# Optimization experiments

Hardware: AMD Instinct MI355X
Metric: run time of the kernel (lower is better)

## Reference

```python
import jax, jax.numpy as jnp
import numpy as np

RES = 64

TRI_TABLE = jnp.array([
    [-1,-1,-1,-1,-1,-1],[1,0,2,-1,-1,-1],[4,0,3,-1,-1,-1],[1,4,2,1,3,4],
    [3,1,5,-1,-1,-1],[2,3,0,2,5,3],[1,4,0,1,5,4],[4,2,5,-1,-1,-1],
    [4,5,2,-1,-1,-1],[4,1,0,4,5,1],[3,2,0,3,5,2],[1,3,5,-1,-1,-1],
    [4,1,2,4,3,1],[3,0,4,-1,-1,-1],[2,0,1,-1,-1,-1],[-1,-1,-1,-1,-1,-1]], dtype=jnp.int32)
NUM_TRI = jnp.array([0,1,1,2,1,2,2,1,1,2,2,1,2,1,1,0], dtype=jnp.int32)
BASE_EDGES = jnp.array([0,1,0,2,0,3,1,2,1,3,2,3], dtype=jnp.int32)


def _make_tet_grid(res):
    # Kuhn 6-tet decomposition of each cube of a (res+1)^3 grid.
    n = res + 1
    ii, jj, kk = np.meshgrid(np.arange(n), np.arange(n), np.arange(n), indexing='ij')
    verts = (np.stack([ii, jj, kk], -1).reshape(-1, 3).astype(np.float32)) / res
    def vid(i, j, k):
        return (i * n + j) * n + k
    i, j, k = np.meshgrid(np.arange(res), np.arange(res), np.arange(res), indexing='ij')
    i, j, k = i.ravel(), j.ravel(), k.ravel()
    c = [vid(i + (b & 1), j + ((b >> 1) & 1), k + ((b >> 2) & 1)) for b in range(8)]
    kuhn = [(0,1,3,7),(0,3,2,7),(0,2,6,7),(0,6,4,7),(0,4,5,7),(0,5,1,7)]
    tets = np.stack([np.stack([c[a], c[b], c[d], c[e]], -1) for (a, b, d, e) in kuhn], 1)
    return verts, tets.reshape(-1, 4).astype(np.int64)


def setup_inputs() -> dict:
    key = jax.random.key(0)
    verts, tets = _make_tet_grid(RES)
    level = jax.random.normal(key, (verts.shape[0], 1), dtype=jnp.float32)
    return {"level": level, "pos": jnp.asarray(verts), "tet": jnp.asarray(tets), "threshold": 0}


def reference(level, pos, tet, threshold):
    sdf = level - threshold                    # [N,1]
    occ = sdf[:, 0] > 0                        # [N]
    occ_fx4 = occ[tet]                         # [F,4]
    occ_sum = occ_fx4.sum(-1)
    valid = (occ_sum > 0) & (occ_sum < 4)
    vt = tet[valid]                            # [Fv,4]
    occ_valid = occ_fx4[valid]                 # [Fv,4]

    edges = jnp.sort(vt[:, BASE_EDGES].reshape(-1, 2), axis=1)   # [Fv*6,2]
    unique_edges, idx_map = jnp.unique(edges, axis=0, return_inverse=True)
    idx_map = idx_map.reshape(-1)
    mask_edges = occ[unique_edges].sum(-1) == 1                  # crossing edges
    mapping = jnp.where(mask_edges, jnp.cumsum(mask_edges) - 1, -1)
    idx_map = mapping[idx_map].reshape(-1, 6)                    # [Fv,6]
    interp_v = unique_edges[mask_edges]                          # [M,2]

    p = pos[interp_v]                                            # [M,2,3]
    s = sdf[interp_v][..., 0] * jnp.array([1.0, -1.0], dtype=sdf.dtype)  # [M,2]
    w = s[:, ::-1] / s.sum(1, keepdims=True)                     # flip / denom
    verts_out = (p * w[..., None]).sum(1)                        # [M,3]

    v_id = 2 ** jnp.arange(4, dtype=jnp.int32)
    tetindex = (occ_valid.astype(jnp.int32) * v_id).sum(-1)      # [Fv]
    num_tri = NUM_TRI[tetindex]
    m1, m2 = num_tri == 1, num_tri == 2
    f1 = jnp.take_along_axis(idx_map[m1], TRI_TABLE[tetindex[m1]][:, :3], axis=1).reshape(-1, 3)
    f2 = jnp.take_along_axis(idx_map[m2], TRI_TABLE[tetindex[m2]][:, :6], axis=1).reshape(-1, 3)
    faces = jnp.concatenate([f1, f2], axis=0)
    return verts_out, faces
```

## Files before the change

kernel.cpp:

```cpp
#include <hip/hip_runtime.h>


#define RESX 64
#define NV   65
#define NV2  4225
#define NVERT 274625
#define BLOCK 256
#define NGE 4225
#define NGC 4096
#define NB1I 1024
#define NBND 129
#define NBLK1 1057
#define CBLK 1024
#define NFB 33
#define STAGE 9216
#define M21 0x1fffffu
#define NTRI_PACK 0x16696994u

__constant__ int c_tri[16][6] = {
    {-1,-1,-1,-1,-1,-1},{1,0,2,-1,-1,-1},{4,0,3,-1,-1,-1},{1,4,2,1,3,4},
    {3,1,5,-1,-1,-1},{2,3,0,2,5,3},{1,4,0,1,5,4},{4,2,5,-1,-1,-1},
    {4,5,2,-1,-1,-1},{4,1,0,4,5,1},{3,2,0,3,5,2},{1,3,5,-1,-1,-1},
    {4,1,2,4,3,1},{3,0,4,-1,-1,-1},{2,0,1,-1,-1,-1},{-1,-1,-1,-1,-1,-1}};
__constant__ int c_kuhn[6][4] = {{0,1,3,7},{0,3,2,7},{0,2,6,7},{0,6,4,7},{0,4,5,7},{0,5,1,7}};
__constant__ int c_off8[8] = {0,4225,65,4290,1,4226,66,4291};
__constant__ int c_loc[6][6] = {
    {0,0,0,1,1,3},{0,0,0,2,3,2},{0,0,0,2,2,6},
    {0,0,0,4,6,4},{0,0,0,4,4,5},{0,0,0,1,5,1}};
__constant__ int c_dir[6][6] = {
    {3,5,6,1,2,0},{5,1,6,3,0,4},{1,2,6,0,4,3},
    {2,0,6,1,3,5},{0,4,6,3,5,1},{4,3,6,0,1,2}};

typedef unsigned long long u64;

__device__ __forceinline__ unsigned block_scan_excl(unsigned val, unsigned* lds,
                                                    unsigned& block_total) {
    int tid = threadIdx.x, lane = tid & 63, w = tid >> 6;
    unsigned x = val;
#pragma unroll
    for (int off = 1; off < 64; off <<= 1) {
        unsigned y = (unsigned)__shfl_up((int)x, off, 64);
        if (lane >= off) x += y;
    }
    if (lane == 63) lds[w] = x;
    __syncthreads();
    if (tid == 0) {
        unsigned s = 0;
#pragma unroll
        for (int i = 0; i < 4; i++) { unsigned t = lds[i]; lds[i + 4] = s; s += t; }
        lds[8] = s;
    }
    __syncthreads();
    block_total = lds[8];
    return x - val + lds[4 + w];
}

__device__ __forceinline__ unsigned wave_excl(unsigned cnt, unsigned& incl) {
    int lane = threadIdx.x & 63;
    unsigned x = cnt;
#pragma unroll
    for (int off = 1; off < 64; off <<= 1) {
        unsigned y = (unsigned)__shfl_up((int)x, off, 64);
        if (lane >= off) x += y;
    }
    incl = x;
    return x - cnt;
}

__device__ __forceinline__ void emit_vtx(unsigned fl, const float lv[8],
                                         float fi, float fj, float fk,
                                         unsigned slot, float* stage) {
    if (!(fl & 0x7fu)) return;
    float v0 = lv[0];
    const float inv = 1.f / 64.f;
    const int d2b[7] = {4, 2, 6, 1, 5, 3, 7};
    float* o = &stage[3u * slot];
#pragma unroll
    for (int d = 0; d < 7; d++) {
        if (fl & (1u << d)) {
            const int b = d2b[d];
            float w1 = v0 * __builtin_amdgcn_rcpf(v0 - lv[b]);
            o[0] = (fi + (float)(b & 1) * w1) * inv;
            o[1] = (fj + (float)((b >> 1) & 1) * w1) * inv;
            o[2] = (fk + (float)((b >> 2) & 1) * w1) * inv;
            o += 3;
        }
    }
}

__global__ void __launch_bounds__(256)
pass1(const float* __restrict__ level, const float* __restrict__ thrp,
      unsigned char* __restrict__ flagsArr, unsigned short* __restrict__ locEx,
      unsigned* __restrict__ bsE, unsigned* __restrict__ bsC) {
    int tid = threadIdx.x, lane = tid & 63, w = tid >> 6;
    int bid = blockIdx.x;
    float thr = thrp[0];
    unsigned fl = 0, fl65 = 0, c1 = 0, c2 = 0;
    int base, grp, cgrp = -1;

    if (bid < NB1I) {
        int ci = bid >> 4, cj = ((bid & 15) << 2) + w;
        grp = ci * NV + cj;
        base = grp * NV;
        int v = base + lane;
        float r0  = level[v]        - thr;
        float rY  = level[v + 65]   - thr;
        float rX  = level[v + 4225] - thr;
        float rXY = level[v + 4290] - thr;
        float t0 = 0.f, tY = 0.f, tX = 0.f, tXY = 0.f;
        if (lane == 63) {
            t0  = level[base + 64]   - thr;
            tY  = level[base + 129]  - thr;
            tX  = level[base + 4289] - thr;
            tXY = level[base + 4354] - thr;
        }
        float a4 = __shfl_down(r0, 1, 64);  if (lane == 63) a4 = t0;
        float a6 = __shfl_down(rY, 1, 64);  if (lane == 63) a6 = tY;
        float a5 = __shfl_down(rX, 1, 64);  if (lane == 63) a5 = tX;
        float a7 = __shfl_down(rXY, 1, 64); if (lane == 63) a7 = tXY;
        bool s0 = r0 > 0.f;
        fl = s0 ? 0x80u : 0u;
        if ((a4  > 0.f) != s0) fl |= 1u;
        if ((rY  > 0.f) != s0) fl |= 2u;
        if ((a6  > 0.f) != s0) fl |= 4u;
        if ((rX  > 0.f) != s0) fl |= 8u;
        if ((a5  > 0.f) != s0) fl |= 16u;
        if ((rXY > 0.f) != s0) fl |= 32u;
        if ((a7  > 0.f) != s0) fl |= 64u;
        unsigned occ8 = (r0  > 0.f ?   1u : 0u) | (rX  > 0.f ?   2u : 0u)
                      | (rY  > 0.f ?   4u : 0u) | (rXY > 0.f ?   8u : 0u)
                      | (a4  > 0.f ?  16u : 0u) | (a5  > 0.f ?  32u : 0u)
                      | (a6  > 0.f ?  64u : 0u) | (a7  > 0.f ? 128u : 0u);
#pragma unroll
        for (int t = 0; t < 6; t++) {
            int cfg = ((occ8 >> c_kuhn[t][0]) & 1) | (((occ8 >> c_kuhn[t][1]) & 1) << 1)
                    | (((occ8 >> c_kuhn[t][2]) & 1) << 2) | (((occ8 >> c_kuhn[t][3]) & 1) << 3);
            unsigned nt = (NTRI_PACK >> (cfg << 1)) & 3u;
            c1 += (nt == 1); c2 += (nt == 2);
        }
        if (lane == 63) {
            bool s65 = t0 > 0.f;
            fl65 = s65 ? 0x80u : 0u;
            if ((tY  > 0.f) != s65) fl65 |= 2u;
            if ((tX  > 0.f) != s65) fl65 |= 8u;
            if ((tXY > 0.f) != s65) fl65 |= 32u;
        }
        cgrp = (ci << 6) + cj;
    } else {
        int bw = (bid - NB1I) * 4 + w;
        if (bw >= NBND) return;
        if (bw < 64) {
            grp = bw * NV + 64;
            base = grp * NV;
            int v = base + lane;
            float r0 = level[v]        - thr;
            float rX = level[v + 4225] - thr;
            float t0 = 0.f, tX = 0.f;
            if (lane == 63) { t0 = level[base + 64] - thr; tX = level[base + 4289] - thr; }
            float a1 = __shfl_down(r0, 1, 64); if (lane == 63) a1 = t0;
            float a5 = __shfl_down(rX, 1, 64); if (lane == 63) a5 = tX;
            bool s0 = r0 > 0.f;
            fl = s0 ? 0x80u : 0u;
            if ((a1 > 0.f) != s0) fl |= 1u;
            if ((rX > 0.f) != s0) fl |= 8u;
            if ((a5 > 0.f) != s0) fl |= 16u;
            if (lane == 63) {
                bool s65 = t0 > 0.f;
                fl65 = s65 ? 0x80u : 0u;
                if ((tX > 0.f) != s65) fl65 |= 8u;
            }
        } else if (bw < 128) {
            int j = bw - 64;
            grp = 64 * NV + j;
            base = grp * NV;
            int v = base + lane;
            float r0 = level[v]      - thr;
            float rY = level[v + 65] - thr;
            float t0 = 0.f, tY = 0.f;
            if (lane == 63) { t0 = level[base + 64] - thr; tY = level[base + 129] - thr; }
            float a1 = __shfl_down(r0, 1, 64); if (lane == 63) a1 = t0;
            float a3 = __shfl_down(rY, 1, 64); if (lane == 63) a3 = tY;
            bool s0 = r0 > 0.f;
            fl = s0 ? 0x80u : 0u;
            if ((a1 > 0.f) != s0) fl |= 1u;
            if ((rY > 0.f) != s0) fl |= 2u;
            if ((a3 > 0.f) != s0) fl |= 4u;
            if (lane == 63) {
                bool s65 = t0 > 0.f;
                fl65 = s65 ? 0x80u : 0u;
                if ((tY > 0.f) != s65) fl65 |= 2u;
            }
        } else {
            grp = 64 * NV + 64;
            base = grp * NV;
            int v = base + lane;
            float r0 = level[v] - thr;
            float t0 = 0.f;
            if (lane == 63) t0 = level[base + 64] - thr;
            float a1 = __shfl_down(r0, 1, 64); if (lane == 63) a1 = t0;
            bool s0 = r0 > 0.f;
            fl = s0 ? 0x80u : 0u;
            if ((a1 > 0.f) != s0) fl |= 1u;
            if (lane == 63) fl65 = (t0 > 0.f) ? 0x80u : 0u;
        }
    }

    unsigned cnt65 = __popc(fl65 & 0x7fu);
    unsigned cnt = __popc(fl & 0x7fu);
    unsigned val = cnt | (c1 << 10) | (c2 << 20);
    unsigned x = val;
#pragma unroll
    for (int off = 1; off < 64; off <<= 1) {
        unsigned y = (unsigned)__shfl_up((int)x, off, 64);
        if (lane >= off) x += y;
    }
    int v = base + lane;
    flagsArr[v] = (unsigned char)fl;
    locEx[v] = (unsigned short)((x - val) & 0x3ffu);
    if (lane == 63) {
        unsigned totE64 = x & 0x3ffu;
        flagsArr[base + 64] = (unsigned char)fl65;
        locEx[base + 64] = (unsigned short)totE64;
        bsE[grp] = totE64 + cnt65;
        if (cgrp >= 0)
            bsC[cgrp] = ((x >> 10) & 0x3ffu) | (((x >> 20) & 0x3ffu) << 16);
    }
}

__global__ void __launch_bounds__(1024)
scanK(const unsigned* __restrict__ bsE, const unsigned* __restrict__ bsC,
      unsigned* __restrict__ preE, uint2* __restrict__ preC) {
    int tid = threadIdx.x, lane = tid & 63, w = tid >> 6;
    if (blockIdx.x == 0) {
        __shared__ unsigned lws[16];
        unsigned ev[5]; unsigned s = 0;
#pragma unroll
        for (int e = 0; e < 5; e++) {
            int idx = tid * 5 + e;
            unsigned a = (idx < NGE) ? bsE[idx] : 0u;
            ev[e] = a; s += a;
        }
        unsigned x = s;
#pragma unroll
        for (int off = 1; off < 64; off <<= 1) {
            unsigned y = (unsigned)__shfl_up((int)x, off, 64);
            if (lane >= off) x += y;
        }
        if (lane == 63) lws[w] = x;
        __syncthreads();
        if (tid == 0) {
            unsigned acc = 0;
#pragma unroll
            for (int i = 0; i < 16; i++) { unsigned t = lws[i]; lws[i] = acc; acc += t; }
        }
        __syncthreads();
        unsigned run = x - s + lws[w];
#pragma unroll
        for (int e = 0; e < 5; e++) {
            int idx = tid * 5 + e;
            if (idx <= NGE) preE[idx] = run;
            run += ev[e];
        }
    } else {
        __shared__ u64 lwc[16];
        u64 cv[4]; u64 cs = 0;
#pragma unroll
        for (int e = 0; e < 4; e++) {
            int idx = tid * 4 + e;
            unsigned a = (idx < NGC) ? bsC[idx] : 0u;
            u64 p = (u64)(a & 0xffffu) | ((u64)(a >> 16) << 21);
            cv[e] = p; cs += p;
        }
        u64 cx = cs;
#pragma unroll
        for (int off = 1; off < 64; off <<= 1) {
            u64 y = __shfl_up(cx, off, 64);
            if (lane >= off) cx += y;
        }
        if (lane == 63) lwc[w] = cx;
        __syncthreads();
        if (tid == 0) {
            u64 acc = 0;
#pragma unroll
            for (int i = 0; i < 16; i++) { u64 t = lwc[i]; lwc[i] = acc; acc += t; }
        }
        __syncthreads();
        u64 crun = cx - cs + lwc[w];
#pragma unroll
        for (int e = 0; e < 4; e++) {
            int idx = tid * 4 + e;
            if (idx < NGC)
                preC[idx] = make_uint2((unsigned)(crun & M21), (unsigned)((crun >> 21) & M21));
            crun += cv[e];
        }
        if (tid == 1023)
            preC[NGC] = make_uint2((unsigned)(crun & M21), (unsigned)((crun >> 21) & M21));
    }
}

__global__ void __launch_bounds__(256)
pass2(const float* __restrict__ level, const float* __restrict__ thrp,
      const unsigned char* __restrict__ flagsArr,
      const unsigned short* __restrict__ locEx,
      const unsigned* __restrict__ preE, const uint2* __restrict__ preC,
      float* __restrict__ out) {
    __shared__ unsigned lds[9];
    __shared__ unsigned pEw[10];
    __shared__ unsigned short rankW[650];
    __shared__ unsigned char flagsW[656];
    __shared__ float stage[STAGE];
    int tid = threadIdx.x, bid = blockIdx.x, lane = tid & 63, w = tid >> 6;
    float thr = thrp[0];
    int ci = bid >> 4, cj0 = (bid & 15) << 2;
    int ccj = cj0 + w;
    int grpA = ci * NV + cj0;
    int grp = grpA + w;
    unsigned pE = preE[grpA];
    unsigned totE_blk = preE[grpA + 4] - pE;
    if (tid < 10) pEw[tid] = preE[(ci + tid / 5) * NV + cj0 + tid % 5];
    for (int idx = tid; idx < 650; idx += BLOCK) {
        int wrow = idx / 65;
        int kk = idx - wrow * 65;
        int di = (wrow >= 5) ? 1 : 0;
        int vid = ((ci + di) * NV + cj0 + wrow - 5 * di) * NV + kk;
        rankW[idx] = locEx[vid];
        flagsW[idx] = flagsArr[vid];
    }

    {
        int vbase = grp * NV;
        int v = vbase + lane;
        float r0  = level[v]        - thr;
        float rY  = level[v + 65]   - thr;
        float rX  = level[v + 4225] - thr;
        float rXY = level[v + 4290] - thr;
        float t0 = 0.f, tY = 0.f, tX = 0.f, tXY = 0.f;
        if (lane == 63) {
            t0  = level[vbase + 64]   - thr;
            tY  = level[vbase + 129]  - thr;
            tX  = level[vbase + 4289] - thr;
            tXY = level[vbase + 4354] - thr;
        }
        float a4 = __shfl_down(r0, 1, 64);  if (lane == 63) a4 = t0;
        float a6 = __shfl_down(rY, 1, 64);  if (lane == 63) a6 = tY;
        float a5 = __shfl_down(rX, 1, 64);  if (lane == 63) a5 = tX;
        float a7 = __shfl_down(rXY, 1, 64); if (lane == 63) a7 = tXY;
        bool s0 = r0 > 0.f;
        unsigned fl = s0 ? 0x80u : 0u;
        if ((a4  > 0.f) != s0) fl |= 1u;
        if ((rY  > 0.f) != s0) fl |= 2u;
        if ((a6  > 0.f) != s0) fl |= 4u;
        if ((rX  > 0.f) != s0) fl |= 8u;
        if ((a5  > 0.f) != s0) fl |= 16u;
        if ((rXY > 0.f) != s0) fl |= 32u;
        if ((a7  > 0.f) != s0) fl |= 64u;
        unsigned cnt = __popc(fl & 0x7fu);
        unsigned incl, wex;
        wex = wave_excl(cnt, incl);
        unsigned slotRow = preE[grp] - pE;
        float lv[8] = {r0, rX, rY, rXY, a4, a5, a6, a7};
        emit_vtx(fl, lv, (float)ci, (float)ccj, (float)lane, slotRow + wex, stage);
        if (lane == 63) {
            bool s65 = t0 > 0.f;
            unsigned fl65 = s65 ? 0x80u : 0u;
            if ((tY  > 0.f) != s65) fl65 |= 2u;
            if ((tX  > 0.f) != s65) fl65 |= 8u;
            if ((tXY > 0.f) != s65) fl65 |= 32u;
            float lv65[8] = {t0, tX, tY, tXY, 0.f, 0.f, 0.f, 0.f};
            emit_vtx(fl65, lv65, (float)ci, (float)ccj, 64.f, slotRow + incl, stage);
        }
    }
    __syncthreads();
    {
        float* dst = out + 3u * pE;
        unsigned n = totE_blk * 3u;
        for (unsigned idx = tid; idx < n; idx += BLOCK)
            __builtin_nontemporal_store(stage[idx], &dst[idx]);
    }

    if (bid < NFB) {
        __syncthreads();
        int bg = 4 * bid + w;
        if (bg < NBND) {
            int i, j;
            if (bg < 64)       { i = bg; j = 64; }
            else if (bg < 128) { i = 64; j = bg - 64; }
            else               { i = 64; j = 64; }
            int vbase = (i * NV + j) * NV;
            int v = vbase + lane;
            float r0 = level[v] - thr;
            float t0 = (lane == 63) ? level[vbase + 64] - thr : 0.f;
            float a1 = __shfl_down(r0, 1, 64); if (lane == 63) a1 = t0;
            bool s0 = r0 > 0.f;
            unsigned fl = s0 ? 0x80u : 0u;
            if ((a1 > 0.f) != s0) fl |= 1u;
            bool s65 = t0 > 0.f;
            unsigned fl65 = s65 ? 0x80u : 0u;
            float lv[8] = {r0, 0.f, 0.f, 0.f, a1, 0.f, 0.f, 0.f};
            float lv65[8] = {t0, 0.f, 0.f, 0.f, 0.f, 0.f, 0.f, 0.f};
            if (bg < 64) {
                float rX = level[v + 4225] - thr;
                float tX = (lane == 63) ? level[vbase + 4289] - thr : 0.f;
                float a5 = __shfl_down(rX, 1, 64); if (lane == 63) a5 = tX;
                if ((rX > 0.f) != s0) fl |= 8u;
                if ((a5 > 0.f) != s0) fl |= 16u;
                lv[1] = rX; lv[5] = a5;
                if ((tX > 0.f) != s65) fl65 |= 8u;
                lv65[1] = tX;
            } else if (bg < 128) {
                float rY = level[v + 65] - thr;
                float tY = (lane == 63) ? level[vbase + 129] - thr : 0.f;
                float a3 = __shfl_down(rY, 1, 64); if (lane == 63) a3 = tY;
                if ((rY > 0.f) != s0) fl |= 2u;
                if ((a3 > 0.f) != s0) fl |= 4u;
                lv[2] = rY; lv[6] = a3;
                if ((tY > 0.f) != s65) fl65 |= 2u;
                lv65[2] = tY;
            }
            unsigned cnt = __popc(fl & 0x7fu);
            unsigned incl, wex;
            wex = wave_excl(cnt, incl);
            float* st = stage + 1365u * (unsigned)w;
            emit_vtx(fl, lv, (float)i, (float)j, (float)lane, wex, st);
            if (lane == 63)
                emit_vtx(fl65, lv65, (float)i, (float)j, 64.f, incl, st);
        }
        __syncthreads();
#pragma unroll
        for (int gsel = 0; gsel < 4; gsel++) {
            int bgf = 4 * bid + gsel;
            if (bgf >= NBND) break;
            int grpB = (bgf < 64) ? bgf * NV + 64 : 64 * NV + (bgf - 64);
            unsigned pg = preE[grpB];
            unsigned n = (preE[grpB + 1] - pg) * 3u;
            float* dst = out + 3u * pg;
            for (unsigned idx = tid; idx < n; idx += BLOCK)
                __builtin_nontemporal_store(stage[1365u * (unsigned)gsel + idx], &dst[idx]);
        }
    }
    __syncthreads();

    int kk = lane;
    u64 f8 = 0ull;
#pragma unroll
    for (int b = 0; b < 8; b++) {
        int widx = 5 * (b & 1) + w + ((b >> 1) & 1);
        f8 |= (u64)flagsW[widx * 65 + kk + ((b >> 2) & 1)] << (8 * b);
    }
    unsigned occ8 = 0;
#pragma unroll
    for (int b = 0; b < 8; b++) occ8 |= (unsigned)((f8 >> (8 * b + 7)) & 1ull) << b;
    int cfgs[6];
    unsigned c1 = 0, c2 = 0;
#pragma unroll
    for (int t = 0; t < 6; t++) {
        int cfg = ((occ8 >> c_kuhn[t][0]) & 1) | (((occ8 >> c_kuhn[t][1]) & 1) << 1)
                | (((occ8 >> c_kuhn[t][2]) & 1) << 2) | (((occ8 >> c_kuhn[t][3]) & 1) << 3);
        cfgs[t] = cfg;
        unsigned nt = (NTRI_PACK >> (cfg << 1)) & 3u;
        c1 += (nt == 1); c2 += (nt == 2);
    }
    unsigned tot2;
    unsigned ex2 = block_scan_excl(c1 | (c2 << 16), lds, tot2);
    unsigned f1 = tot2 & 0xffffu;
    unsigned f2 = tot2 >> 16;
    unsigned l1c = ex2 & 0xffffu;
    unsigned l2c = ex2 >> 16;
    unsigned n1 = f1 * 3u;
#pragma unroll
    for (int t = 0; t < 6; t++) {
        int cfg = cfgs[t];
        unsigned nt = (NTRI_PACK >> (cfg << 1)) & 3u;
        if (nt == 0) continue;
        auto rank = [&](int e) -> float {
            int lc = c_loc[t][e];
            int dir = c_dir[t][e];
            int widx = 5 * (lc & 1) + w + ((lc >> 1) & 1);
            int lidx = widx * 65 + kk + ((lc >> 2) & 1);
            unsigned flb = (unsigned)((f8 >> (8 * lc)) & 0xffull);
            return (float)(pEw[widx] + rankW[lidx] + __popc(flb & ((1u << dir) - 1u)));
        };
        float ra = rank(c_tri[cfg][0]);
        float rb = rank(c_tri[cfg][1]);
        float rc = rank(c_tri[cfg][2]);
        if (nt == 1) {
            unsigned bfo = 3u * l1c;
            stage[bfo] = ra; stage[bfo + 1] = rb; stage[bfo + 2] = rc;
            l1c++;
        } else {
            float rd = rank(c_tri[cfg][4]);
            unsigned bfo = n1 + 6u * l2c;
            stage[bfo]     = ra; stage[bfo + 1] = rb; stage[bfo + 2] = rc;
            stage[bfo + 3] = ra; stage[bfo + 4] = rd; stage[bfo + 5] = rb;
            l2c++;
        }
    }
    __syncthreads();
    unsigned M = preE[NGE];
    unsigned C1 = preC[NGC].x;
    uint2 pc = preC[4 * bid];
    float* of = out + 3ull * M;
    float* o1 = of + 3u * pc.x;
    for (unsigned idx = tid; idx < n1; idx += BLOCK)
        __builtin_nontemporal_store(stage[idx], &o1[idx]);
    unsigned n2 = f2 * 6u;
    float* o2 = of + 3u * (C1 + 2u * pc.y);
    for (unsigned idx = tid; idx < n2; idx += BLOCK)
        __builtin_nontemporal_store(stage[n1 + idx], &o2[idx]);
}

extern "C" void kernel_launch(void* const* d_in, const int* in_sizes, int n_in,
                              void* d_out, int out_size, void* d_ws, size_t ws_size,
                              hipStream_t stream) {
    const float* level = (const float*)d_in[0];
    const float* thrp = (const float*)d_in[3];
    float* out = (float*)d_out;

    char* p = (char*)d_ws;
    unsigned char* flagsArr = (unsigned char*)p;
    p += (NVERT + 255) & ~255;
    unsigned short* locEx = (unsigned short*)p;
    p += ((sizeof(unsigned short) * NVERT) + 255) & ~255;
    unsigned* bsE = (unsigned*)p;
    p += ((sizeof(unsigned) * NGE) + 255) & ~255;
    unsigned* bsC = (unsigned*)p;
    p += ((sizeof(unsigned) * NGC) + 255) & ~255;
    unsigned* preE = (unsigned*)p;
    p += ((sizeof(unsigned) * (NGE + 1)) + 255) & ~255;
    uint2* preC = (uint2*)p;

    pass1<<<NBLK1, BLOCK, 0, stream>>>(level, thrp, flagsArr, locEx, bsE, bsC);
    scanK<<<2, 1024, 0, stream>>>(bsE, bsC, preE, preC);
    pass2<<<CBLK, BLOCK, 0, stream>>>(level, thrp, flagsArr, locEx, preE, preC, out);
}
```

Baseline: 106.3 us.

## Remove scan kernel; compute block prefixes redundantly inside pass2 via reductions

Drops the separate two-block scanK launch. Each pass2 block now reads the whole bsE and bsC arrays and reduces them to get its own exclusive prefixes, the totals, and the boundary-group offsets. These are packed into 64-bit values with 21-bit fields. This removes one kernel launch and the serialised scan stage between pass1 and pass2. In exchange, every one of the 1024 blocks does redundant global reads of about 8K words and runs extra block reductions with syncs.

```diff
diff --git a/kernel.cpp b/kernel.cpp
--- a/kernel.cpp
+++ b/kernel.cpp
@@ -32,6 +32,18 @@
     {2,0,6,1,3,5},{0,4,6,3,5,1},{4,3,6,0,1,2}};
 
 typedef unsigned long long u64;
+
+__device__ __forceinline__ u64 block_reduce_u64(u64 v, u64* lds) {
+    int tid = threadIdx.x, lane = tid & 63, w = tid >> 6;
+#pragma unroll
+    for (int off = 32; off > 0; off >>= 1)
+        v += __shfl_xor(v, off, 64);
+    if (lane == 0) lds[w] = v;
+    __syncthreads();
+    if (tid == 0) lds[4] = lds[0] + lds[1] + lds[2] + lds[3];
+    __syncthreads();
+    return lds[4];
+}
 
 __device__ __forceinline__ unsigned block_scan_excl(unsigned val, unsigned* lds,
                                                     unsigned& block_total) {
@@ -227,85 +239,16 @@
     }
 }
 
-__global__ void __launch_bounds__(1024)
-scanK(const unsigned* __restrict__ bsE, const unsigned* __restrict__ bsC,
-      unsigned* __restrict__ preE, uint2* __restrict__ preC) {
-    int tid = threadIdx.x, lane = tid & 63, w = tid >> 6;
-    if (blockIdx.x == 0) {
-        __shared__ unsigned lws[16];
-        unsigned ev[5]; unsigned s = 0;
-#pragma unroll
-        for (int e = 0; e < 5; e++) {
-            int idx = tid * 5 + e;
-            unsigned a = (idx < NGE) ? bsE[idx] : 0u;
-            ev[e] = a; s += a;
-        }
-        unsigned x = s;
-#pragma unroll
-        for (int off = 1; off < 64; off <<= 1) {
-            unsigned y = (unsigned)__shfl_up((int)x, off, 64);
-            if (lane >= off) x += y;
-        }
-        if (lane == 63) lws[w] = x;
-        __syncthreads();
-        if (tid == 0) {
-            unsigned acc = 0;
-#pragma unroll
-            for (int i = 0; i < 16; i++) { unsigned t = lws[i]; lws[i] = acc; acc += t; }
-        }
-        __syncthreads();
-        unsigned run = x - s + lws[w];
-#pragma unroll
-        for (int e = 0; e < 5; e++) {
-            int idx = tid * 5 + e;
-            if (idx <= NGE) preE[idx] = run;
-            run += ev[e];
-        }
-    } else {
-        __shared__ u64 lwc[16];
-        u64 cv[4]; u64 cs = 0;
-#pragma unroll
-        for (int e = 0; e < 4; e++) {
-            int idx = tid * 4 + e;
-            unsigned a = (idx < NGC) ? bsC[idx] : 0u;
-            u64 p = (u64)(a & 0xffffu) | ((u64)(a >> 16) << 21);
-            cv[e] = p; cs += p;
-        }
-        u64 cx = cs;
-#pragma unroll
-        for (int off = 1; off < 64; off <<= 1) {
-            u64 y = __shfl_up(cx, off, 64);
-            if (lane >= off) cx += y;
-        }
-        if (lane == 63) lwc[w] = cx;
-        __syncthreads();
-        if (tid == 0) {
-            u64 acc = 0;
-#pragma unroll
-            for (int i = 0; i < 16; i++) { u64 t = lwc[i]; lwc[i] = acc; acc += t; }
-        }
-        __syncthreads();
-        u64 crun = cx - cs + lwc[w];
-#pragma unroll
-        for (int e = 0; e < 4; e++) {
-            int idx = tid * 4 + e;
-            if (idx < NGC)
-                preC[idx] = make_uint2((unsigned)(crun & M21), (unsigned)((crun >> 21) & M21));
-            crun += cv[e];
-        }
-        if (tid == 1023)
-            preC[NGC] = make_uint2((unsigned)(crun & M21), (unsigned)((crun >> 21) & M21));
-    }
-}
-
 __global__ void __launch_bounds__(256)
 pass2(const float* __restrict__ level, const float* __restrict__ thrp,
       const unsigned char* __restrict__ flagsArr,
       const unsigned short* __restrict__ locEx,
-      const unsigned* __restrict__ preE, const uint2* __restrict__ preC,
+      const unsigned* __restrict__ bsE, const unsigned* __restrict__ bsC,
       float* __restrict__ out) {
     __shared__ unsigned lds[9];
+    __shared__ u64 lds64[5];
     __shared__ unsigned pEw[10];
+    __shared__ unsigned pBs[4], nBs[4];
     __shared__ unsigned short rankW[650];
     __shared__ unsigned char flagsW[656];
     __shared__ float stage[STAGE];
@@ -314,10 +257,9 @@
     int ci = bid >> 4, cj0 = (bid & 15) << 2;
     int ccj = cj0 + w;
     int grpA = ci * NV + cj0;
+    int grpA2 = grpA + NV;
     int grp = grpA + w;
-    unsigned pE = preE[grpA];
-    unsigned totE_blk = preE[grpA + 4] - pE;
-    if (tid < 10) pEw[tid] = preE[(ci + tid / 5) * NV + cj0 + tid % 5];
+
     for (int idx = tid; idx < 650; idx += BLOCK) {
         int wrow = idx / 65;
         int kk = idx - wrow * 65;
@@ -326,6 +268,66 @@
         rankW[idx] = locEx[vid];
         flagsW[idx] = flagsArr[vid];
     }
+
+    unsigned sE0 = 0, sE1 = 0, sEt = 0;
+    for (int t = tid; t < NGE; t += BLOCK) {
+        unsigned a = bsE[t];
+        sEt += a;
+        if (t < grpA)  sE0 += a;
+        if (t < grpA2) sE1 += a;
+    }
+    unsigned sC1 = 0, sC2 = 0, sC1t = 0;
+    int cpre = 4 * bid;
+    for (int t = tid; t < NGC; t += BLOCK) {
+        unsigned a = bsC[t];
+        unsigned a1 = a & 0xffffu, a2 = a >> 16;
+        sC1t += a1;
+        if (t < cpre) { sC1 += a1; sC2 += a2; }
+    }
+    u64 rE = block_reduce_u64((u64)sE0 | ((u64)sE1 << 21) | ((u64)sEt << 42), lds64);
+    u64 rC = block_reduce_u64((u64)sC1 | ((u64)sC2 << 21) | ((u64)sC1t << 42), lds64);
+    unsigned pE  = (unsigned)rE & M21;
+    unsigned A1  = (unsigned)(rE >> 21) & M21;
+    unsigned M   = (unsigned)(rE >> 42);
+    unsigned p1b = (unsigned)rC & M21;
+    unsigned p2b = (unsigned)(rC >> 21) & M21;
+    unsigned C1  = (unsigned)(rC >> 42);
+    bool hasB = (bid < NFB);
+    if (hasB) {
+        int gb[4]; unsigned sB[4] = {0, 0, 0, 0};
+#pragma unroll
+        for (int g = 0; g < 4; g++) {
+            int bg = 4 * bid + g;
+            gb[g] = (bg >= NBND) ? 0 : (bg < 64 ? bg * NV + 64 : bg + 4096);
+        }
+        for (int t = tid; t < NGE; t += BLOCK) {
+            unsigned a = bsE[t];
+#pragma unroll
+            for (int g = 0; g < 4; g++)
+                if (t < gb[g]) sB[g] += a;
+        }
+        u64 rB0 = block_reduce_u64((u64)sB[0] | ((u64)sB[1] << 21) | ((u64)sB[2] << 42), lds64);
+        u64 rB1 = block_reduce_u64((u64)sB[3], lds64);
+        if (tid < 4) {
+            unsigned pb = (tid == 0) ? ((unsigned)rB0 & M21)
+                        : (tid == 1) ? ((unsigned)(rB0 >> 21) & M21)
+                        : (tid == 2) ? ((unsigned)(rB0 >> 42))
+                                     : ((unsigned)rB1 & M21);
+            pBs[tid] = pb;
+            nBs[tid] = (4 * bid + tid < NBND) ? bsE[gb[tid]] : 0u;
+        }
+    }
+    if (tid < 2) {
+        unsigned run = (tid == 0) ? pE : A1;
+        int rbase = (tid == 0) ? grpA : grpA2;
+#pragma unroll
+        for (int d = 0; d < 5; d++) {
+            pEw[5 * tid + d] = run;
+            if (d < 4) run += bsE[rbase + d];
+        }
+    }
+    __syncthreads();
+    unsigned totE_blk = pEw[4] - pE;
 
     {
         int vbase = grp * NV;
@@ -357,7 +359,7 @@
         unsigned cnt = __popc(fl & 0x7fu);
         unsigned incl, wex;
         wex = wave_excl(cnt, incl);
-        unsigned slotRow = preE[grp] - pE;
+        unsigned slotRow = pEw[w] - pE;
         float lv[8] = {r0, rX, rY, rXY, a4, a5, a6, a7};
         emit_vtx(fl, lv, (float)ci, (float)ccj, (float)lane, slotRow + wex, stage);
         if (lane == 63) {
@@ -378,7 +380,7 @@
             __builtin_nontemporal_store(stage[idx], &dst[idx]);
     }
 
-    if (bid < NFB) {
+    if (hasB) {
         __syncthreads();
         int bg = 4 * bid + w;
         if (bg < NBND) {
@@ -430,9 +432,8 @@
         for (int gsel = 0; gsel < 4; gsel++) {
             int bgf = 4 * bid + gsel;
             if (bgf >= NBND) break;
-            int grpB = (bgf < 64) ? bgf * NV + 64 : 64 * NV + (bgf - 64);
-            unsigned pg = preE[grpB];
-            unsigned n = (preE[grpB + 1] - pg) * 3u;
+            unsigned pg = pBs[gsel];
+            unsigned n = nBs[gsel] * 3u;
             float* dst = out + 3u * pg;
             for (unsigned idx = tid; idx < n; idx += BLOCK)
                 __builtin_nontemporal_store(stage[1365u * (unsigned)gsel + idx], &dst[idx]);
@@ -496,15 +497,12 @@
         }
     }
     __syncthreads();
-    unsigned M = preE[NGE];
-    unsigned C1 = preC[NGC].x;
-    uint2 pc = preC[4 * bid];
     float* of = out + 3ull * M;
-    float* o1 = of + 3u * pc.x;
+    float* o1 = of + 3u * p1b;
     for (unsigned idx = tid; idx < n1; idx += BLOCK)
         __builtin_nontemporal_store(stage[idx], &o1[idx]);
     unsigned n2 = f2 * 6u;
-    float* o2 = of + 3u * (C1 + 2u * pc.y);
+    float* o2 = of + 3u * (C1 + 2u * p2b);
     for (unsigned idx = tid; idx < n2; idx += BLOCK)
         __builtin_nontemporal_store(stage[n1 + idx], &o2[idx]);
 }
@@ -524,12 +522,7 @@
     unsigned* bsE = (unsigned*)p;
     p += ((sizeof(unsigned) * NGE) + 255) & ~255;
     unsigned* bsC = (unsigned*)p;
-    p += ((sizeof(unsigned) * NGC) + 255) & ~255;
-    unsigned* preE = (unsigned*)p;
-    p += ((sizeof(unsigned) * (NGE + 1)) + 255) & ~255;
-    uint2* preC = (uint2*)p;
 
     pass1<<<NBLK1, BLOCK, 0, stream>>>(level, thrp, flagsArr, locEx, bsE, bsC);
-    scanK<<<2, 1024, 0, stream>>>(bsE, bsC, preE, preC);
-    pass2<<<CBLK, BLOCK, 0, stream>>>(level, thrp, flagsArr, locEx, preE, preC, out);
-}
+    pass2<<<CBLK, BLOCK, 0, stream>>>(level, thrp, flagsArr, locEx, bsE, bsC, out);
+}
```

New measurement: 108.8 us. 2.4% more time.

## Halve pass2 work per block to double grid size and raise occupancy

Applied to the files above, without the earlier changes.

pass2 now handles two cube rows per block instead of four and launches 2048 blocks. This halves the shared staging buffer, and launch bounds request 8 blocks per CU, so the aim is more resident waves and better latency hiding. The face classification and block scan now run before the vertex store loop, letting stores overlap that work. In exchange, half the threads sit idle in the compute phases, every block does more sync and prefix-load overhead, and the tighter register cap could cause spills.

```diff
diff --git a/kernel.cpp b/kernel.cpp
--- a/kernel.cpp
+++ b/kernel.cpp
@@ -11,9 +11,9 @@
 #define NB1I 1024
 #define NBND 129
 #define NBLK1 1057
-#define CBLK 1024
-#define NFB 33
-#define STAGE 9216
+#define CBLK2 2048
+#define NFB2 65
+#define STAGE2 4608
 #define M21 0x1fffffu
 #define NTRI_PACK 0x16696994u
 
@@ -298,36 +298,35 @@
     }
 }
 
-__global__ void __launch_bounds__(256)
+__global__ void __launch_bounds__(256, 8)
 pass2(const float* __restrict__ level, const float* __restrict__ thrp,
       const unsigned char* __restrict__ flagsArr,
       const unsigned short* __restrict__ locEx,
       const unsigned* __restrict__ preE, const uint2* __restrict__ preC,
       float* __restrict__ out) {
+    __shared__ float stage[STAGE2];
+    __shared__ unsigned short rankW[390];
+    __shared__ unsigned char flagsW[392];
+    __shared__ unsigned pEw[6];
     __shared__ unsigned lds[9];
-    __shared__ unsigned pEw[10];
-    __shared__ unsigned short rankW[650];
-    __shared__ unsigned char flagsW[656];
-    __shared__ float stage[STAGE];
     int tid = threadIdx.x, bid = blockIdx.x, lane = tid & 63, w = tid >> 6;
     float thr = thrp[0];
-    int ci = bid >> 4, cj0 = (bid & 15) << 2;
-    int ccj = cj0 + w;
+    int ci = bid >> 5, cj0 = (bid & 31) << 1;
     int grpA = ci * NV + cj0;
-    int grp = grpA + w;
     unsigned pE = preE[grpA];
-    unsigned totE_blk = preE[grpA + 4] - pE;
-    if (tid < 10) pEw[tid] = preE[(ci + tid / 5) * NV + cj0 + tid % 5];
-    for (int idx = tid; idx < 650; idx += BLOCK) {
+    unsigned totE_blk = preE[grpA + 2] - pE;
+    if (tid < 6) pEw[tid] = preE[(ci + tid / 3) * NV + cj0 + tid % 3];
+    for (int idx = tid; idx < 390; idx += BLOCK) {
         int wrow = idx / 65;
         int kk = idx - wrow * 65;
-        int di = (wrow >= 5) ? 1 : 0;
-        int vid = ((ci + di) * NV + cj0 + wrow - 5 * di) * NV + kk;
+        int di = (wrow >= 3) ? 1 : 0;
+        int vid = ((ci + di) * NV + cj0 + wrow - 3 * di) * NV + kk;
         rankW[idx] = locEx[vid];
         flagsW[idx] = flagsArr[vid];
     }
 
-    {
+    if (w < 2) {
+        int grp = grpA + w;
         int vbase = grp * NV;
         int v = vbase + lane;
         float r0  = level[v]        - thr;
@@ -359,7 +358,8 @@
         wex = wave_excl(cnt, incl);
         unsigned slotRow = preE[grp] - pE;
         float lv[8] = {r0, rX, rY, rXY, a4, a5, a6, a7};
-        emit_vtx(fl, lv, (float)ci, (float)ccj, (float)lane, slotRow + wex, stage);
+        emit_vtx(fl, lv, (float)ci, (float)(cj0 + w), (float)lane,
+                 slotRow + wex, stage);
         if (lane == 63) {
             bool s65 = t0 > 0.f;
             unsigned fl65 = s65 ? 0x80u : 0u;
@@ -367,10 +367,42 @@
             if ((tX  > 0.f) != s65) fl65 |= 8u;
             if ((tXY > 0.f) != s65) fl65 |= 32u;
             float lv65[8] = {t0, tX, tY, tXY, 0.f, 0.f, 0.f, 0.f};
-            emit_vtx(fl65, lv65, (float)ci, (float)ccj, 64.f, slotRow + incl, stage);
+            emit_vtx(fl65, lv65, (float)ci, (float)(cj0 + w), 64.f,
+                     slotRow + incl, stage);
         }
     }
     __syncthreads();
+
+    int ck = lane;
+    int cw = w & 1;
+    u64 f8 = 0ull;
+    int cfgs[6];
+    unsigned c1 = 0, c2 = 0;
+    if (tid < 128) {
+#pragma unroll
+        for (int b = 0; b < 8; b++) {
+            int widx = 3 * (b & 1) + cw + ((b >> 1) & 1);
+            f8 |= (u64)flagsW[widx * 65 + ck + ((b >> 2) & 1)] << (8 * b);
+        }
+        unsigned occ8 = 0;
+#pragma unroll
+        for (int b = 0; b < 8; b++)
+            occ8 |= (unsigned)((f8 >> (8 * b + 7)) & 1ull) << b;
+#pragma unroll
+        for (int t = 0; t < 6; t++) {
+            int cfg = ((occ8 >> c_kuhn[t][0]) & 1) | (((occ8 >> c_kuhn[t][1]) & 1) << 1)
+                    | (((occ8 >> c_kuhn[t][2]) & 1) << 2) | (((occ8 >> c_kuhn[t][3]) & 1) << 3);
+            cfgs[t] = cfg;
+            unsigned nt = (NTRI_PACK >> (cfg << 1)) & 3u;
+            c1 += (nt == 1); c2 += (nt == 2);
+        }
+    } else {
+#pragma unroll
+        for (int t = 0; t < 6; t++) cfgs[t] = 0;
+    }
+    unsigned tot2;
+    unsigned ex2 = block_scan_excl(c1 | (c2 << 16), lds, tot2);
+
     {
         float* dst = out + 3u * pE;
         unsigned n = totE_blk * 3u;
@@ -378,10 +410,10 @@
             __builtin_nontemporal_store(stage[idx], &dst[idx]);
     }
 
-    if (bid < NFB) {
+    if (bid < NFB2) {
         __syncthreads();
-        int bg = 4 * bid + w;
-        if (bg < NBND) {
+        int bg = 2 * bid + w;
+        if (w < 2 && bg < NBND) {
             int i, j;
             if (bg < 64)       { i = bg; j = 64; }
             else if (bg < 128) { i = 64; j = bg - 64; }
@@ -427,78 +459,58 @@
         }
         __syncthreads();
 #pragma unroll
-        for (int gsel = 0; gsel < 4; gsel++) {
-            int bgf = 4 * bid + gsel;
+        for (int g = 0; g < 2; g++) {
+            int bgf = 2 * bid + g;
             if (bgf >= NBND) break;
             int grpB = (bgf < 64) ? bgf * NV + 64 : 64 * NV + (bgf - 64);
             unsigned pg = preE[grpB];
             unsigned n = (preE[grpB + 1] - pg) * 3u;
             float* dst = out + 3u * pg;
             for (unsigned idx = tid; idx < n; idx += BLOCK)
-                __builtin_nontemporal_store(stage[1365u * (unsigned)gsel + idx], &dst[idx]);
+                __builtin_nontemporal_store(stage[1365u * (unsigned)g + idx], &dst[idx]);
         }
     }
     __syncthreads();
 
-    int kk = lane;
-    u64 f8 = 0ull;
-#pragma unroll
-    for (int b = 0; b < 8; b++) {
-        int widx = 5 * (b & 1) + w + ((b >> 1) & 1);
-        f8 |= (u64)flagsW[widx * 65 + kk + ((b >> 2) & 1)] << (8 * b);
-    }
-    unsigned occ8 = 0;
-#pragma unroll
-    for (int b = 0; b < 8; b++) occ8 |= (unsigned)((f8 >> (8 * b + 7)) & 1ull) << b;
-    int cfgs[6];
-    unsigned c1 = 0, c2 = 0;
-#pragma unroll
-    for (int t = 0; t < 6; t++) {
-        int cfg = ((occ8 >> c_kuhn[t][0]) & 1) | (((occ8 >> c_kuhn[t][1]) & 1) << 1)
-                | (((occ8 >> c_kuhn[t][2]) & 1) << 2) | (((occ8 >> c_kuhn[t][3]) & 1) << 3);
-        cfgs[t] = cfg;
-        unsigned nt = (NTRI_PACK >> (cfg << 1)) & 3u;
-        c1 += (nt == 1); c2 += (nt == 2);
-    }
-    unsigned tot2;
-    unsigned ex2 = block_scan_excl(c1 | (c2 << 16), lds, tot2);
     unsigned f1 = tot2 & 0xffffu;
     unsigned f2 = tot2 >> 16;
-    unsigned l1c = ex2 & 0xffffu;
-    unsigned l2c = ex2 >> 16;
     unsigned n1 = f1 * 3u;
-#pragma unroll
-    for (int t = 0; t < 6; t++) {
-        int cfg = cfgs[t];
-        unsigned nt = (NTRI_PACK >> (cfg << 1)) & 3u;
-        if (nt == 0) continue;
-        auto rank = [&](int e) -> float {
-            int lc = c_loc[t][e];
-            int dir = c_dir[t][e];
-            int widx = 5 * (lc & 1) + w + ((lc >> 1) & 1);
-            int lidx = widx * 65 + kk + ((lc >> 2) & 1);
-            unsigned flb = (unsigned)((f8 >> (8 * lc)) & 0xffull);
-            return (float)(pEw[widx] + rankW[lidx] + __popc(flb & ((1u << dir) - 1u)));
-        };
-        float ra = rank(c_tri[cfg][0]);
-        float rb = rank(c_tri[cfg][1]);
-        float rc = rank(c_tri[cfg][2]);
-        if (nt == 1) {
-            unsigned bfo = 3u * l1c;
-            stage[bfo] = ra; stage[bfo + 1] = rb; stage[bfo + 2] = rc;
-            l1c++;
-        } else {
-            float rd = rank(c_tri[cfg][4]);
-            unsigned bfo = n1 + 6u * l2c;
-            stage[bfo]     = ra; stage[bfo + 1] = rb; stage[bfo + 2] = rc;
-            stage[bfo + 3] = ra; stage[bfo + 4] = rd; stage[bfo + 5] = rb;
-            l2c++;
+    if (tid < 128) {
+        unsigned l1c = ex2 & 0xffffu;
+        unsigned l2c = ex2 >> 16;
+#pragma unroll
+        for (int t = 0; t < 6; t++) {
+            int cfg = cfgs[t];
+            unsigned nt = (NTRI_PACK >> (cfg << 1)) & 3u;
+            if (nt == 0) continue;
+            auto rank = [&](int e) -> float {
+                int lc = c_loc[t][e];
+                int dir = c_dir[t][e];
+                int widx = 3 * (lc & 1) + cw + ((lc >> 1) & 1);
+                int lidx = widx * 65 + ck + ((lc >> 2) & 1);
+                unsigned flb = (unsigned)((f8 >> (8 * lc)) & 0xffull);
+                return (float)(pEw[widx] + rankW[lidx] + __popc(flb & ((1u << dir) - 1u)));
+            };
+            float ra = rank(c_tri[cfg][0]);
+            float rb = rank(c_tri[cfg][1]);
+            float rc = rank(c_tri[cfg][2]);
+            if (nt == 1) {
+                unsigned bfo = 3u * l1c;
+                stage[bfo] = ra; stage[bfo + 1] = rb; stage[bfo + 2] = rc;
+                l1c++;
+            } else {
+                float rd = rank(c_tri[cfg][4]);
+                unsigned bfo = n1 + 6u * l2c;
+                stage[bfo]     = ra; stage[bfo + 1] = rb; stage[bfo + 2] = rc;
+                stage[bfo + 3] = ra; stage[bfo + 4] = rd; stage[bfo + 5] = rb;
+                l2c++;
+            }
         }
     }
     __syncthreads();
     unsigned M = preE[NGE];
     unsigned C1 = preC[NGC].x;
-    uint2 pc = preC[4 * bid];
+    uint2 pc = preC[2 * bid];
     float* of = out + 3ull * M;
     float* o1 = of + 3u * pc.x;
     for (unsigned idx = tid; idx < n1; idx += BLOCK)
@@ -531,5 +543,5 @@
 
     pass1<<<NBLK1, BLOCK, 0, stream>>>(level, thrp, flagsArr, locEx, bsE, bsC);
     scanK<<<2, 1024, 0, stream>>>(bsE, bsC, preE, preC);
-    pass2<<<CBLK, BLOCK, 0, stream>>>(level, thrp, flagsArr, locEx, preE, preC, out);
-}
+    pass2<<<CBLK2, BLOCK, 0, stream>>>(level, thrp, flagsArr, locEx, preE, preC, out);
+}
```

New measurement: 105.4 us, median of 2. No clear change (-0.8%).

## Stage face output in two half-block passes to shrink LDS staging buffer

Applied to the files above, without the earlier changes.

Face-writing staging is split into two passes, each covering half the threads (128 per pass), so the LDS staging buffer drops from 9216 to 5460 floats. The midpoint of the block scan (lds[6]) supplies each half's offsets. The smaller LDS footprint may allow more resident blocks per CU. In exchange it adds two extra barriers and serialises the staging work of the two halves. It depends on block_scan_excl leaving the partial sum for the first half in lds[6].

```diff
diff --git a/kernel.cpp b/kernel.cpp
--- a/kernel.cpp
+++ b/kernel.cpp
@@ -13,7 +13,7 @@
 #define NBLK1 1057
 #define CBLK 1024
 #define NFB 33
-#define STAGE 9216
+#define STAGE 5460
 #define M21 0x1fffffu
 #define NTRI_PACK 0x16696994u
 
@@ -462,51 +462,64 @@
     }
     unsigned tot2;
     unsigned ex2 = block_scan_excl(c1 | (c2 << 16), lds, tot2);
-    unsigned f1 = tot2 & 0xffffu;
-    unsigned f2 = tot2 >> 16;
-    unsigned l1c = ex2 & 0xffffu;
-    unsigned l2c = ex2 >> 16;
-    unsigned n1 = f1 * 3u;
-#pragma unroll
-    for (int t = 0; t < 6; t++) {
-        int cfg = cfgs[t];
-        unsigned nt = (NTRI_PACK >> (cfg << 1)) & 3u;
-        if (nt == 0) continue;
-        auto rank = [&](int e) -> float {
-            int lc = c_loc[t][e];
-            int dir = c_dir[t][e];
-            int widx = 5 * (lc & 1) + w + ((lc >> 1) & 1);
-            int lidx = widx * 65 + kk + ((lc >> 2) & 1);
-            unsigned flb = (unsigned)((f8 >> (8 * lc)) & 0xffull);
-            return (float)(pEw[widx] + rankW[lidx] + __popc(flb & ((1u << dir) - 1u)));
-        };
-        float ra = rank(c_tri[cfg][0]);
-        float rb = rank(c_tri[cfg][1]);
-        float rc = rank(c_tri[cfg][2]);
-        if (nt == 1) {
-            unsigned bfo = 3u * l1c;
-            stage[bfo] = ra; stage[bfo + 1] = rb; stage[bfo + 2] = rc;
-            l1c++;
-        } else {
-            float rd = rank(c_tri[cfg][4]);
-            unsigned bfo = n1 + 6u * l2c;
-            stage[bfo]     = ra; stage[bfo + 1] = rb; stage[bfo + 2] = rc;
-            stage[bfo + 3] = ra; stage[bfo + 4] = rd; stage[bfo + 5] = rb;
-            l2c++;
-        }
-    }
-    __syncthreads();
-    unsigned M = preE[NGE];
+    unsigned chunkMid = lds[6];
+    unsigned f1  = tot2 & 0xffffu,  f2  = tot2 >> 16;
+    unsigned f1a = chunkMid & 0xffffu, f2a = chunkMid >> 16;
+    unsigned l1c = ex2 & 0xffffu,  l2c = ex2 >> 16;
+    unsigned M  = preE[NGE];
     unsigned C1 = preC[NGC].x;
     uint2 pc = preC[4 * bid];
     float* of = out + 3ull * M;
     float* o1 = of + 3u * pc.x;
-    for (unsigned idx = tid; idx < n1; idx += BLOCK)
-        __builtin_nontemporal_store(stage[idx], &o1[idx]);
-    unsigned n2 = f2 * 6u;
     float* o2 = of + 3u * (C1 + 2u * pc.y);
-    for (unsigned idx = tid; idx < n2; idx += BLOCK)
-        __builtin_nontemporal_store(stage[n1 + idx], &o2[idx]);
+
+#pragma unroll
+    for (int h = 0; h < 2; h++) {
+        unsigned b1 = h ? f1a : 0u, e1 = h ? f1 : f1a;
+        unsigned b2 = h ? f2a : 0u, e2 = h ? f2 : f2a;
+        unsigned n1c = (e1 - b1) * 3u;
+        if ((tid >> 7) == h) {
+            unsigned m1 = l1c - b1;
+            unsigned m2 = l2c - b2;
+#pragma unroll
+            for (int t = 0; t < 6; t++) {
+                int cfg = cfgs[t];
+                unsigned nt = (NTRI_PACK >> (cfg << 1)) & 3u;
+                if (nt == 0) continue;
+                auto rank = [&](int e) -> float {
+                    int lc = c_loc[t][e];
+                    int dir = c_dir[t][e];
+                    int widx = 5 * (lc & 1) + w + ((lc >> 1) & 1);
+                    int lidx = widx * 65 + kk + ((lc >> 2) & 1);
+                    unsigned flb = (unsigned)((f8 >> (8 * lc)) & 0xffull);
+                    return (float)(pEw[widx] + rankW[lidx] + __popc(flb & ((1u << dir) - 1u)));
+                };
+                float ra = rank(c_tri[cfg][0]);
+                float rb = rank(c_tri[cfg][1]);
+                float rc = rank(c_tri[cfg][2]);
+                if (nt == 1) {
+                    unsigned bfo = 3u * m1;
+                    stage[bfo] = ra; stage[bfo + 1] = rb; stage[bfo + 2] = rc;
+                    m1++;
+                } else {
+                    float rd = rank(c_tri[cfg][4]);
+                    unsigned bfo = n1c + 6u * m2;
+                    stage[bfo]     = ra; stage[bfo + 1] = rb; stage[bfo + 2] = rc;
+                    stage[bfo + 3] = ra; stage[bfo + 4] = rd; stage[bfo + 5] = rb;
+                    m2++;
+                }
+            }
+        }
+        __syncthreads();
+        float* d1 = o1 + 3u * b1;
+        for (unsigned idx = tid; idx < n1c; idx += BLOCK)
+            __builtin_nontemporal_store(stage[idx], &d1[idx]);
+        unsigned n2c = (e2 - b2) * 6u;
+        float* d2 = o2 + 6u * b2;
+        for (unsigned idx = tid; idx < n2c; idx += BLOCK)
+            __builtin_nontemporal_store(stage[n1c + idx], &d2[idx]);
+        __syncthreads();
+    }
 }
 
 extern "C" void kernel_launch(void* const* d_in, const int* in_sizes, int n_in,
```

New measurement: 107.0 us. About the same (+0.7%).
